# Kernel optimization log

Measured on AMD Instinct MI355X. Metric: run time of the kernel, lower is better.

## Reference

```python
import jax, jax.numpy as jnp
import numpy as np

EPS = 1e-5
HEADS = 8  # heads kwarg of TransformerDecoder


def _ln(x, g, b):
    mu = jnp.mean(x, axis=-1, keepdims=True)
    var = jnp.var(x, axis=-1, keepdims=True)
    return (x - mu) * jax.lax.rsqrt(var + EPS) * g + b


def _expert(params, xt, m, scale):
    """One TransformerDecoder expert (BIT-style): per layer, PreNorm2 cross-attn + residual,
    then PreNorm FeedForward + residual. xt: (B,S,D), m: (B,Nt,D)."""
    an_g, an_b, wq, wk, wv, wo, wo_b, fn_g, fn_b, w1, b1, w2, b2 = params
    L = an_g.shape[0]
    B, S, D = xt.shape
    Nt = m.shape[1]
    for l in range(L):
        xn = _ln(xt, an_g[l], an_b[l])
        mn = _ln(m, an_g[l], an_b[l])  # PreNorm2 norms both streams with the same LN
        q = (xn @ wq[l]).reshape(B, S, HEADS, -1)
        k = (mn @ wk[l]).reshape(B, Nt, HEADS, -1)
        v = (mn @ wv[l]).reshape(B, Nt, HEADS, -1)
        attn = jax.nn.softmax(jnp.einsum('bihd,bjhd->bhij', q, k) * scale, axis=-1)
        o = jnp.einsum('bhij,bjhd->bihd', attn, v).reshape(B, S, -1)
        xt = xt + o @ wo[l] + wo_b[l]
        h = _ln(xt, fn_g[l], fn_b[l])
        xt = xt + jax.nn.gelu(h @ w1[l] + b1[l], approximate=False) @ w2[l] + b2[l]
    return xt


def setup_inputs():
    key = jax.random.key(0)
    ks = iter(jax.random.split(key, 40))
    B, C, H, W = 4, 128, 64, 64
    D, INNER, FF, P, L, NT = 256, 512, 1024, 4, 2, 8
    r = lambda shape, s=1.0: jax.random.normal(next(ks), shape, jnp.float32) * s
    return {
        'x': r((B, C, H, W)),
        'm': r((B, NT, D)),
        'proj_w': r((C, D), 0.05), 'proj_b': r((D,), 0.02),
        'lnp_g': jnp.ones((D,), jnp.float32), 'lnp_b': jnp.zeros((D,), jnp.float32),
        'sq_w': r((D, D), 0.05), 'sq_b': r((D,), 0.02),
        'sk_w': r((D, D), 0.05), 'sk_b': r((D,), 0.02),
        'sv_w': r((D, 1), 0.05), 'sv_b': r((1,), 0.02),
        'an_g': jnp.ones((P, L, D), jnp.float32), 'an_b': jnp.zeros((P, L, D), jnp.float32),
        'wq': r((P, L, D, INNER), 0.05), 'wk': r((P, L, D, INNER), 0.05), 'wv': r((P, L, D, INNER), 0.05),
        'wo': r((P, L, INNER, D), 0.05), 'wo_b': r((P, L, D), 0.02),
        'fn_g': jnp.ones((P, L, D), jnp.float32), 'fn_b': jnp.zeros((P, L, D), jnp.float32),
        'w1': r((P, L, D, FF), 0.05), 'b1': r((P, L, FF), 0.02),
        'w2': r((P, L, FF, D), 0.05), 'b2': r((P, L, D), 0.02),
        'fln_g': jnp.ones((D,), jnp.float32), 'fln_b': jnp.zeros((D,), jnp.float32),
    }


def reference(x, m, proj_w, proj_b, lnp_g, lnp_b, sq_w, sq_b, sk_w, sk_b, sv_w, sv_b,
              an_g, an_b, wq, wk, wv, wo, wo_b, fn_g, fn_b, w1, b1, w2, b2, fln_g, fln_b):
    B, C, H, W = x.shape
    D = proj_w.shape[1]
    # 1x1 conv -> flatten(2).transpose(1,2): row-major (h,w) tokens
    tokens = jnp.einsum('bchw,cd->bhwd', x, proj_w).reshape(B, H * W, D) + proj_b
    tokens = _ln(tokens, lnp_g, lnp_b)
    # TokenScorer: cross-attention importance scores, v projects to scalar
    q = tokens @ sq_w + sq_b
    k = m @ sk_w + sk_b
    v = m @ sv_w + sv_b  # (B, Nt, 1)
    aw = jax.nn.softmax(jnp.einsum('bnd,bmd->bnm', q, k) / jnp.sqrt(jnp.float32(D)), axis=-1)
    scores = jnp.einsum('bnm,bmo->bno', aw, v)[..., 0]  # (B, N)
    P = an_g.shape[0]
    N = tokens.shape[1]
    S = N // P
    # descending sort of token scores
    idx = jnp.argsort(-scores, axis=1)  # (B, N)
    pscores = jnp.take_along_axis(scores, idx, axis=1).reshape(B, P, S).mean(-1)  # (B, P)
    pw = jax.nn.softmax(pscores, axis=1)  # (B, P)
    # gather tokens per partition: (P, B, S, D)
    gathered = jnp.take_along_axis(tokens, idx[..., None], axis=1).reshape(B, P, S, D).transpose(1, 0, 2, 3)
    scale = 1.0 / jnp.sqrt(jnp.float32(D))  # Cross_Attention scale = dim ** -0.5
    params = (an_g, an_b, wq, wk, wv, wo, wo_b, fn_g, fn_b, w1, b1, w2, b2)
    proc = jax.vmap(lambda pr, xt: _expert(pr, xt, m, scale))(params, gathered)  # (P, B, S, D)
    proc = proc * pw.T[:, :, None, None]
    flat = proc.transpose(1, 0, 2, 3).reshape(B, N, D)
    # scatter back into original token order (idx is a permutation)
    out = jnp.zeros_like(tokens).at[jnp.arange(B)[:, None], idx].set(flat)
    return _ln(out, fln_g, fln_b)
```

## Files before the change

### kernel.cpp

```cpp
#include <hip/hip_runtime.h>
#include <hip/hip_bf16.h>
#include <math.h>

#define BB 4
#define CC 128
#define NN 4096
#define DD 256
#define INNER 512
#define FFD 1024
#define PP 4
#define LL 2
#define NT 8
#define SS 1024
#define SCALE 0.0625f

typedef __attribute__((ext_vector_type(8))) short bf16x8;
typedef __attribute__((ext_vector_type(8))) short short8;
typedef __attribute__((ext_vector_type(4))) short short4v;
typedef __attribute__((ext_vector_type(4))) float f32x4;

#define GLD_LDS16(g, l) __builtin_amdgcn_global_load_lds( \
    (const __attribute__((address_space(1))) void*)(g), \
    (__attribute__((address_space(3))) void*)(l), 16, 0, 0)

template<int NW>
__device__ inline float block_sum(float v, float* sbuf){
  #pragma unroll
  for (int mk=32; mk; mk>>=1) v += __shfl_xor(v, mk);
  int w = threadIdx.x>>6;
  if ((threadIdx.x&63)==0) sbuf[w]=v;
  __syncthreads();
  float r = 0.f;
  #pragma unroll
  for (int k=0;k<NW;k++) r += sbuf[k];
  __syncthreads();
  return r;
}

__device__ inline unsigned short bf16bits(float v){
  __hip_bfloat16 t = __float2bfloat16(v);
  unsigned short u;
  __builtin_memcpy(&u, &t, 2);
  return u;
}
__device__ inline float bf2f(unsigned short u){
  unsigned int x = ((unsigned int)u)<<16;
  float f;
  __builtin_memcpy(&f, &x, 4);
  return f;
}

__device__ inline float gelu_f(float x){
  float z  = x * 0.70710678118654752440f;
  float az = fabsf(z);
  float t  = 1.0f / (1.0f + 0.3275911f*az);
  float y  = t*(0.254829592f + t*(-0.284496736f + t*(1.421413741f +
             t*(-1.453152027f + t*1.061405429f))));
  float erfv = 1.0f - y*__expf(-az*az);
  erfv = (z < 0.0f) ? -erfv : erfv;
  return 0.5f*x*(1.0f+erfv);
}

__global__ __launch_bounds__(256) void prep_kernel(
    const float* __restrict__ m, const float* __restrict__ sk_w,
    const float* __restrict__ sk_b, const float* __restrict__ sv_w,
    const float* __restrict__ sv_b, const float* __restrict__ sq_w,
    const float* __restrict__ sq_b,
    float* __restrict__ kk2, float* __restrict__ kb, float* __restrict__ vsc,
    const float* __restrict__ an_g, const float* __restrict__ an_b,
    const float* __restrict__ wk, const float* __restrict__ wv,
    float* __restrict__ kvk, float* __restrict__ kvv,
    const float* __restrict__ wq, const float* __restrict__ w1,
    const float* __restrict__ w2,
    __hip_bfloat16* __restrict__ wqT, __hip_bfloat16* __restrict__ w1T,
    __hip_bfloat16* __restrict__ w2T)
{
  __shared__ float smem[64*65];
  int z = blockIdx.x;
  int tid = threadIdx.x;
  if (z < 32){
    float* ms = smem;
    float* ks = smem + 256;
    float* sbuf = smem + 512;
    int bj = z;
    ms[tid] = m[bj*DD + tid];
    __syncthreads();
    float acc=0.f;
    #pragma unroll 8
    for(int c=0;c<DD;c++) acc = fmaf(ms[c], sk_w[c*DD + tid], acc);
    ks[tid] = acc + sk_b[tid];
    float sv = block_sum<4>(ms[tid]*sv_w[tid], sbuf);
    if(tid==0) vsc[bj] = sv + sv_b[0];
    __syncthreads();
    const float* wr = sq_w + (long)tid*DD;
    float a2 = 0.f;
    #pragma unroll 4
    for (int c=0; c<DD; c+=4){
      float4 wvv = *(const float4*)(wr + c);
      a2 = fmaf(wvv.x, ks[c+0], fmaf(wvv.y, ks[c+1], fmaf(wvv.z, ks[c+2], fmaf(wvv.w, ks[c+3], a2))));
    }
    kk2[bj*DD + tid] = a2;
    float kbv = block_sum<4>(sq_b[tid]*ks[tid], sbuf);
    if (tid==0) kb[bj] = kbv;
  } else if (z < 288){
    float* mn = smem;
    float* sbuf = smem + 256;
    int idx = z - 32;
    int j = idx & 7, b = (idx>>3)&3, pl = idx>>5;
    float v = m[(b*NT+j)*DD + tid];
    float s = block_sum<4>(v, sbuf);
    float mu = s*(1.0f/256.0f);
    float dv = v-mu;
    float q = block_sum<4>(dv*dv, sbuf);
    float rs = rsqrtf(q*(1.0f/256.0f)+1e-5f);
    mn[tid] = dv*rs*an_g[pl*DD+tid] + an_b[pl*DD+tid];
    __syncthreads();
    float ka0=0.f, va0=0.f, ka1=0.f, va1=0.f;
    const float* wkb = wk + (long)pl*DD*INNER;
    const float* wvb = wv + (long)pl*DD*INNER;
    #pragma unroll 8
    for (int c=0;c<DD;c++){
      float mc = mn[c];
      const float* wkr = wkb + (long)c*INNER;
      const float* wvr = wvb + (long)c*INNER;
      ka0 = fmaf(mc, wkr[tid], ka0);
      ka1 = fmaf(mc, wkr[tid+256], ka1);
      va0 = fmaf(mc, wvr[tid], va0);
      va1 = fmaf(mc, wvr[tid+256], va1);
    }
    long off = ((long)pl*BB + b)*(NT*INNER) + j*INNER;
    kvk[off+tid]=ka0; kvk[off+tid+256]=ka1;
    kvv[off+tid]=va0; kvv[off+tid+256]=va1;
  } else {
    int z2 = z - 288;
    const float* src; __hip_bfloat16* dst; int K, N, rel;
    if (z2 < 256)      { src=wq; dst=wqT; K=DD;   N=INNER; rel=z2; }
    else if (z2 < 768) { src=w1; dst=w1T; K=DD;   N=FFD;   rel=z2-256; }
    else               { src=w2; dst=w2T; K=FFD;  N=DD;    rel=z2-768; }
    int tn = N>>6, tk = K>>6, per = tn*tk;
    int pl = rel/per, r2 = rel%per;
    int n0 = (r2%tn)*64, k0 = (r2/tn)*64;
    float (*t)[65] = (float(*)[65])smem;
    #pragma unroll
    for (int i=0;i<4;i++){
      int idx = i*256+tid;
      int kk = idx>>4, n4 = idx&15;
      float4 v = *(const float4*)&src[((long)pl*K + k0+kk)*N + n0 + n4*4];
      t[kk][n4*4+0]=v.x; t[kk][n4*4+1]=v.y; t[kk][n4*4+2]=v.z; t[kk][n4*4+3]=v.w;
    }
    __syncthreads();
    #pragma unroll
    for (int i=0;i<4;i++){
      int idx = i*256+tid;
      int nn = idx>>4, k4 = idx&15;
      short4v o;
      o[0] = (short)bf16bits(t[k4*4+0][nn]);
      o[1] = (short)bf16bits(t[k4*4+1][nn]);
      o[2] = (short)bf16bits(t[k4*4+2][nn]);
      o[3] = (short)bf16bits(t[k4*4+3][nn]);
      *(short4v*)&dst[((long)pl*N + n0+nn)*K + k0 + k4*4] = o;
    }
  }
}

__global__ __launch_bounds__(256) void proj_ln_score_kernel(
    const float* __restrict__ x, const float* __restrict__ proj_w,
    const float* __restrict__ proj_b, const float* __restrict__ lnp_g,
    const float* __restrict__ lnp_b, const float* __restrict__ kk2,
    const float* __restrict__ kb, const float* __restrict__ vsc,
    float* __restrict__ tokens, float* __restrict__ scores,
    int* __restrict__ rank, long long* __restrict__ psumsI)
{
  int b  = blockIdx.x >> 8;
  int n0 = (blockIdx.x & 255) * 16;
  int tid = threadIdx.x;
  __shared__ float xs[16][132];
  __shared__ float ys[16][260];
  __shared__ float kj[8][260];
  __shared__ float kbs[8], vs[8];
  __shared__ float mu_s[16], rs_s[16];
  __shared__ float lg[16][8];
  if (tid < 16) rank[b*NN + n0 + tid] = 0;
  if (blockIdx.x == 0 && tid < 16) psumsI[tid] = 0;
  #pragma unroll
  for (int i=0;i<8;i++){
    int l = tid + i*256;
    int t = l & 15, c = l >> 4;
    xs[t][c] = x[(long)(b*CC + c)*NN + n0 + t];
  }
  #pragma unroll
  for (int i=0;i<8;i++){
    int idx = i*256 + tid;
    int r = idx >> 8, c = idx & 255;
    kj[r][c] = kk2[(b*NT + r)*DD + c];
  }
  if (tid < 8){ kbs[tid] = kb[b*NT+tid]; vs[tid] = vsc[b*NT+tid]; }
  __syncthreads();
  float acc[16];
  #pragma unroll
  for (int t=0;t<16;t++) acc[t]=0.f;
  for (int c0=0;c0<CC;c0+=4){
    float w0 = proj_w[(c0+0)*DD + tid];
    float w1_ = proj_w[(c0+1)*DD + tid];
    float w2_ = proj_w[(c0+2)*DD + tid];
    float w3_ = proj_w[(c0+3)*DD + tid];
    #pragma unroll
    for (int t=0;t<16;t++){
      float4 xv = *(const float4*)&xs[t][c0];
      acc[t] = fmaf(xv.x,w0,fmaf(xv.y,w1_,fmaf(xv.z,w2_,fmaf(xv.w,w3_,acc[t]))));
    }
  }
  float pb = proj_b[tid];
  #pragma unroll
  for (int t=0;t<16;t++) ys[t][tid] = acc[t] + pb;
  __syncthreads();
  int w = tid>>6, lane = tid&63;
  for (int k=0;k<4;k++){
    int t = w*4+k;
    float s = ys[t][lane] + ys[t][lane+64] + ys[t][lane+128] + ys[t][lane+192];
    #pragma unroll
    for (int mk=32; mk; mk>>=1) s += __shfl_xor(s, mk);
    float mu = s*(1.0f/256.0f);
    float d0=ys[t][lane]-mu, d1=ys[t][lane+64]-mu, d2=ys[t][lane+128]-mu, d3=ys[t][lane+192]-mu;
    float q = d0*d0+d1*d1+d2*d2+d3*d3;
    #pragma unroll
    for (int mk=32; mk; mk>>=1) q += __shfl_xor(q, mk);
    if (lane==0){ mu_s[t]=mu; rs_s[t]=rsqrtf(q*(1.0f/256.0f)+1e-5f); }
  }
  __syncthreads();
  float g = lnp_g[tid], be = lnp_b[tid];
  #pragma unroll
  for (int t=0;t<16;t++){
    float nv = (ys[t][tid]-mu_s[t])*rs_s[t]*g + be;
    tokens[((long)(b*NN + n0 + t))*DD + tid] = nv;
    ys[t][tid] = nv;
  }
  __syncthreads();
  if (tid < 128){
    int t = tid>>3, j = tid&7;
    float a2 = 0.f;
    for (int c0=0;c0<DD;c0+=4){
      float4 tv = *(const float4*)&ys[t][c0];
      float4 kv = *(const float4*)&kj[j][c0];
      a2 = fmaf(tv.x,kv.x,fmaf(tv.y,kv.y,fmaf(tv.z,kv.z,fmaf(tv.w,kv.w,a2))));
    }
    lg[t][j] = (a2 + kbs[j]) * SCALE;
  }
  __syncthreads();
  if (tid < 16){
    float mx=-1e30f;
    #pragma unroll
    for(int j=0;j<NT;j++) mx=fmaxf(mx,lg[tid][j]);
    float s=0.f, sc=0.f;
    #pragma unroll
    for(int j=0;j<NT;j++){ float e=__expf(lg[tid][j]-mx); s+=e; sc+=e*vs[j]; }
    scores[b*NN + n0 + tid] = sc/s;
  }
}

__global__ __launch_bounds__(256) void rank_partial_kernel(
    const float* __restrict__ scores, int* __restrict__ rank)
{
  int b  = blockIdx.x >> 8;
  int it = (blockIdx.x >> 4) & 15;
  int jt = blockIdx.x & 15;
  int i = it*256 + threadIdx.x;
  float si = scores[b*NN + i];
  __shared__ float ss[256];
  ss[threadIdx.x] = scores[b*NN + jt*256 + threadIdx.x];
  __syncthreads();
  int jbase = jt*256;
  int cnt = 0;
  #pragma unroll 4
  for (int j=0;j<256;j++){
    float sj = ss[j];
    cnt += (sj > si) || (sj == si && (jbase+j) < i);
  }
  atomicAdd(&rank[b*NN+i], cnt);
}

__global__ __launch_bounds__(256) void rank_finalize_kernel(
    const int* __restrict__ rank, const float* __restrict__ scores,
    int* __restrict__ cidx, long long* __restrict__ psumsI)
{
  __shared__ unsigned long long bins[PP];
  if (threadIdx.x < PP) bins[threadIdx.x] = 0ull;
  __syncthreads();
  int b = blockIdx.x >> 4;
  int i = (blockIdx.x & 15)*256 + threadIdx.x;
  int rk = rank[b*NN + i];
  int p = rk >> 10;
  cidx[(b*PP + p)*SS + (rk & (SS-1))] = i;
  long long iv = (long long)llrintf(scores[b*NN + i] * 268435456.0f);
  atomicAdd(&bins[p], (unsigned long long)iv);
  __syncthreads();
  if (threadIdx.x < PP)
    atomicAdd((unsigned long long*)&psumsI[b*PP + threadIdx.x], bins[threadIdx.x]);
}

__global__ __launch_bounds__(256) void gather_ln_kernel(
    const float* __restrict__ tokens, const int* __restrict__ cidx,
    float* __restrict__ Xc, __hip_bfloat16* __restrict__ Y,
    const float* __restrict__ gamma, const float* __restrict__ beta)
{
  long slot = (long)blockIdx.x*8 + (threadIdx.x>>5);
  int l32 = threadIdx.x & 31;
  int b = (int)(slot >> 12);
  int p = (int)((slot>>10)&3);
  int i = cidx[slot];
  const float* src = tokens + ((long)b*NN + i)*DD + l32*8;
  float4 v0 = *(const float4*)src;
  float4 v1 = *(const float4*)(src+4);
  *(float4*)(Xc + slot*DD + l32*8) = v0;
  *(float4*)(Xc + slot*DD + l32*8 + 4) = v1;
  float s = v0.x+v0.y+v0.z+v0.w+v1.x+v1.y+v1.z+v1.w;
  #pragma unroll
  for (int mk=16; mk; mk>>=1) s += __shfl_xor(s, mk);
  float mu = s*(1.0f/256.0f);
  float vv[8] = {v0.x,v0.y,v0.z,v0.w,v1.x,v1.y,v1.z,v1.w};
  float q = 0.f;
  #pragma unroll
  for (int k=0;k<8;k++){ float d = vv[k]-mu; q += d*d; }
  #pragma unroll
  for (int mk=16; mk; mk>>=1) q += __shfl_xor(q, mk);
  float rs = rsqrtf(q*(1.0f/256.0f)+1e-5f);
  short8 o;
  #pragma unroll
  for (int k=0;k<8;k++){
    int d = l32*8+k;
    o[k] = (short)bf16bits((vv[k]-mu)*rs*gamma[p*(LL*DD)+d]+beta[p*(LL*DD)+d]);
  }
  *(short8*)(Y + slot*DD + l32*8) = o;
}

__global__ __launch_bounds__(256) void qkvwo_kernel(
    const float* __restrict__ kvk, const float* __restrict__ kvv,
    const __hip_bfloat16* __restrict__ wqT, const float* __restrict__ wo,
    __hip_bfloat16* __restrict__ qkBuf, __hip_bfloat16* __restrict__ vwoT)
{
  int zz = blockIdx.x;
  int z = zz>>3, h = zz&7;
  int l = z>>4, g = z&15;
  int b = g>>2, p = g&3;
  int pl = p*LL + l;
  int c = threadIdx.x;
  __shared__ float kL[8][64];
  __shared__ float vL[8][64];
  {
    int j0 = c>>6, d0 = c&63;
    long off = ((long)pl*BB + b)*(NT*INNER) + h*64 + d0;
    kL[j0][d0]   = kvk[off + j0*INNER];
    vL[j0][d0]   = kvv[off + j0*INNER];
    kL[j0+4][d0] = kvk[off + (j0+4)*INNER];
    vL[j0+4][d0] = kvv[off + (j0+4)*INNER];
  }
  __syncthreads();
  float qa[8] = {0,0,0,0,0,0,0,0};
  float va[8] = {0,0,0,0,0,0,0,0};
  const __hip_bfloat16* wqp = wqT + ((long)pl*INNER + h*64)*DD + c;
  const float* wop = wo + ((long)pl*INNER + h*64)*DD + c;
  #pragma unroll 4
  for (int d=0; d<64; d++){
    float wqv = bf2f(*(const unsigned short*)(wqp + (long)d*DD));
    float wov = wop[(long)d*DD];
    #pragma unroll
    for (int j=0;j<8;j++){
      qa[j] = fmaf(kL[j][d], wqv, qa[j]);
      va[j] = fmaf(vL[j][d], wov, va[j]);
    }
  }
  __hip_bfloat16* qkg = qkBuf + (long)z*64*256;
  __hip_bfloat16* vwg = vwoT + (long)z*256*64;
  #pragma unroll
  for (int j=0;j<8;j++)
    qkg[(h*8+j)*256 + c] = __float2bfloat16(qa[j]*SCALE);
  short8 o;
  #pragma unroll
  for (int j=0;j<8;j++) o[j] = (short)bf16bits(va[j]);
  *(short8*)(vwg + c*64 + h*8) = o;
}

template<bool HASBIAS, bool GELU, bool ACCUM>
__global__ __launch_bounds__(256) void mfma_gemm(
    const __hip_bfloat16* __restrict__ A, long astride, int K,
    const __hip_bfloat16* __restrict__ BT, long bpstride,
    const float* __restrict__ bias, int bias_pstride,
    void* __restrict__ Cp, int ldc, long cstride)
{
  int g = blockIdx.z;
  int p = g & 3;
  const __hip_bfloat16* Ag = A  + (long)g*astride + (long)blockIdx.x*128*K;
  const __hip_bfloat16* Bg = BT + (long)p*bpstride + (long)blockIdx.y*128*K;
  const float* biasg = HASBIAS ? (bias + (long)p*bias_pstride) : nullptr;

  __shared__ __align__(16) __hip_bfloat16 Asm[2][128*64];
  __shared__ __align__(16) __hip_bfloat16 Bsm[2][128*64];

  int tid = threadIdx.x;
  int w = tid>>6, lane = tid&63;
  int wr = w>>1, wc = w&1;
  int lr = lane>>4, lc = lane&15;
  int ldsbase = tid & ~63;

  const __hip_bfloat16* aseg[4];
  const __hip_bfloat16* bseg[4];
  #pragma unroll
  for (int i=0;i<4;i++){
    int seg = i*256 + tid;
    int r = seg>>3, sl = seg&7;
    int sg = sl ^ (r&7);
    aseg[i] = Ag + (long)r*K + sg*8;
    bseg[i] = Bg + (long)r*K + sg*8;
  }

  f32x4 acc[4][4] = {};
  int nt = K >> 6;

  #define STAGE(buf) do { \
    _Pragma("unroll") \
    for (int i_=0;i_<4;i_++) \
      GLD_LDS16(aseg[i_], &Asm[buf][(i_*256 + ldsbase)*8]); \
    _Pragma("unroll") \
    for (int i_=0;i_<4;i_++) \
      GLD_LDS16(bseg[i_], &Bsm[buf][(i_*256 + ldsbase)*8]); \
    _Pragma("unroll") \
    for (int i_=0;i_<4;i_++){ aseg[i_] += 64; bseg[i_] += 64; } \
  } while(0)

  STAGE(0);
  asm volatile("s_waitcnt vmcnt(0)" ::: "memory");
  __syncthreads();

  for (int t=0; t<nt; t++){
    int cur = t & 1;
    if (t+1 < nt) STAGE(cur^1);
    #pragma unroll
    for (int kc=0;kc<2;kc++){
      bf16x8 af[4], bfr[4];
      #pragma unroll
      for (int mi=0;mi<4;mi++){
        int r = wr*64 + mi*16 + lc;
        int s = kc*4 + lr;
        af[mi] = *(const bf16x8*)(&Asm[cur][r*64 + (s ^ (r&7))*8]);
      }
      #pragma unroll
      for (int ni=0;ni<4;ni++){
        int r = wc*64 + ni*16 + lc;
        int s = kc*4 + lr;
        bfr[ni] = *(const bf16x8*)(&Bsm[cur][r*64 + (s ^ (r&7))*8]);
      }
      #pragma unroll
      for (int mi=0;mi<4;mi++)
        #pragma unroll
        for (int ni=0;ni<4;ni++)
          acc[mi][ni] = __builtin_amdgcn_mfma_f32_16x16x32_bf16(af[mi], bfr[ni], acc[mi][ni], 0, 0, 0);
    }
    if (t+1 < nt) asm volatile("s_waitcnt vmcnt(0)" ::: "memory");
    __syncthreads();
  }
  #undef STAGE

  if (ACCUM){
    float* Cg = (float*)Cp + (long)g*cstride;
    #pragma unroll
    for (int ni=0;ni<4;ni++){
      int col = blockIdx.y*128 + wc*64 + ni*16 + lc;
      float bv = HASBIAS ? biasg[col] : 0.0f;
      #pragma unroll
      for (int mi=0;mi<4;mi++){
        int row = blockIdx.x*128 + wr*64 + mi*16 + lr*4;
        #pragma unroll
        for (int j=0;j<4;j++){
          float v = acc[mi][ni][j] + bv;
          if (GELU) v = gelu_f(v);
          Cg[(long)(row+j)*ldc + col] += v;
        }
      }
    }
  } else {
    __hip_bfloat16* Cg = (__hip_bfloat16*)Cp + (long)g*cstride;
    #pragma unroll
    for (int ni=0;ni<4;ni++){
      int col = blockIdx.y*128 + wc*64 + ni*16 + lc;
      float bv = HASBIAS ? biasg[col] : 0.0f;
      #pragma unroll
      for (int mi=0;mi<4;mi++){
        int row = blockIdx.x*128 + wr*64 + mi*16 + lr*4;
        #pragma unroll
        for (int j=0;j<4;j++){
          float v = acc[mi][ni][j] + bv;
          if (GELU) v = gelu_f(v);
          Cg[(long)(row+j)*ldc + col] = __float2bfloat16(v);
        }
      }
    }
  }
}

template<bool LAST>
__global__ __launch_bounds__(256) void ff2_fused_kernel(
    const __hip_bfloat16* __restrict__ F,
    const __hip_bfloat16* __restrict__ w2l,
    const float* __restrict__ b2l,
    float* __restrict__ Xc,
    const float* __restrict__ g_ln,
    const float* __restrict__ b_ln,
    __hip_bfloat16* __restrict__ actOut,
    const int* __restrict__ cidx,
    const long long* __restrict__ psumsI,
    float* __restrict__ out)
{
  int rb = blockIdx.x;
  int g  = blockIdx.y;
  int p  = g & 3;
  const __hip_bfloat16* Ag = F + ((long)g*SS + rb*64)*FFD;
  const __hip_bfloat16* Bg = w2l + (long)p*((long)LL*DD*FFD);

  __shared__ __align__(16) __hip_bfloat16 As[2][64*64];
  __shared__ __align__(16) __hip_bfloat16 Bs[2][256*64];

  int tid = threadIdx.x;
  int w = tid>>6, lane = tid&63;
  int lr = lane>>4, lc = lane&15;
  int ldsbase = tid & ~63;

  const __hip_bfloat16* aseg[2];
  const __hip_bfloat16* bseg[8];
  #pragma unroll
  for (int i=0;i<2;i++){
    int seg = i*256 + tid;
    int r = seg>>3, sl = seg&7;
    aseg[i] = Ag + (long)r*FFD + (sl ^ (r&7))*8;
  }
  #pragma unroll
  for (int i=0;i<8;i++){
    int seg = i*256 + tid;
    int r = seg>>3, sl = seg&7;
    bseg[i] = Bg + (long)r*FFD + (sl ^ (r&7))*8;
  }

  f32x4 acc[4][4] = {};

  #define STAGE2(buf) do { \
    _Pragma("unroll") \
    for (int i_=0;i_<2;i_++) \
      GLD_LDS16(aseg[i_], &As[buf][(i_*256 + ldsbase)*8]); \
    _Pragma("unroll") \
    for (int i_=0;i_<8;i_++) \
      GLD_LDS16(bseg[i_], &Bs[buf][(i_*256 + ldsbase)*8]); \
    _Pragma("unroll") \
    for (int i_=0;i_<2;i_++) aseg[i_] += 64; \
    _Pragma("unroll") \
    for (int i_=0;i_<8;i_++) bseg[i_] += 64; \
  } while(0)

  STAGE2(0);
  asm volatile("s_waitcnt vmcnt(0)" ::: "memory");
  __syncthreads();

  for (int t=0; t<16; t++){
    int cur = t & 1;
    if (t+1 < 16) STAGE2(cur^1);
    #pragma unroll
    for (int kc=0;kc<2;kc++){
      bf16x8 af[4], bfr[4];
      #pragma unroll
      for (int mi=0;mi<4;mi++){
        int r = mi*16 + lc;
        int s = kc*4 + lr;
        af[mi] = *(const bf16x8*)(&As[cur][r*64 + (s ^ (r&7))*8]);
      }
      #pragma unroll
      for (int ni=0;ni<4;ni++){
        int c = w*64 + ni*16 + lc;
        int s = kc*4 + lr;
        bfr[ni] = *(const bf16x8*)(&Bs[cur][c*64 + (s ^ (c&7))*8]);
      }
      #pragma unroll
      for (int mi=0;mi<4;mi++)
        #pragma unroll
        for (int ni=0;ni<4;ni++)
          acc[mi][ni] = __builtin_amdgcn_mfma_f32_16x16x32_bf16(af[mi], bfr[ni], acc[mi][ni], 0, 0, 0);
    }
    if (t+1 < 16) asm volatile("s_waitcnt vmcnt(0)" ::: "memory");
    __syncthreads();
  }
  #undef STAGE2

  __syncthreads();
  float* pfl = (float*)&As[0][0];
  float* pfq = (float*)&As[0][0] + 256;
  float* Xg = Xc + (long)g*SS*DD + (long)rb*64*DD;

  float pwv = 1.0f;
  if (LAST){
    int b = g>>2;
    float ps[4];
    #pragma unroll
    for (int p2=0;p2<4;p2++)
      ps[p2] = (float)((double)psumsI[b*PP+p2] * (1.0/268435456.0/1024.0));
    float mxp = fmaxf(fmaxf(ps[0],ps[1]),fmaxf(ps[2],ps[3]));
    float e0=__expf(ps[0]-mxp), e1=__expf(ps[1]-mxp), e2=__expf(ps[2]-mxp), e3=__expf(ps[3]-mxp);
    float es = e0+e1+e2+e3;
    float ev = (p==0)?e0:(p==1)?e1:(p==2)?e2:e3;
    pwv = ev/es;
  }

  float srow[4][4], qrow[4][4];
  #pragma unroll
  for (int mi=0;mi<4;mi++)
    #pragma unroll
    for (int j=0;j<4;j++){ srow[mi][j]=0.f; qrow[mi][j]=0.f; }
  #pragma unroll
  for (int ni=0;ni<4;ni++){
    int col = w*64 + ni*16 + lc;
    float bv = b2l[p*(LL*DD) + col];
    #pragma unroll
    for (int mi=0;mi<4;mi++){
      int row = mi*16 + lr*4;
      #pragma unroll
      for (int j=0;j<4;j++){
        float v = Xg[(long)(row+j)*DD + col] + acc[mi][ni][j] + bv;
        if (!LAST) Xg[(long)(row+j)*DD + col] = v;
        if (LAST) v *= pwv;
        acc[mi][ni][j] = v;
        srow[mi][j] += v;
        qrow[mi][j] += v*v;
      }
    }
  }
  #pragma unroll
  for (int mi=0;mi<4;mi++)
    #pragma unroll
    for (int j=0;j<4;j++){
      float s2=srow[mi][j], q2=qrow[mi][j];
      s2 += __shfl_xor(s2,1); q2 += __shfl_xor(q2,1);
      s2 += __shfl_xor(s2,2); q2 += __shfl_xor(q2,2);
      s2 += __shfl_xor(s2,4); q2 += __shfl_xor(q2,4);
      s2 += __shfl_xor(s2,8); q2 += __shfl_xor(q2,8);
      srow[mi][j]=s2; qrow[mi][j]=q2;
    }
  if (lc==0){
    #pragma unroll
    for (int mi=0;mi<4;mi++)
      #pragma unroll
      for (int j=0;j<4;j++){
        int row = mi*16 + lr*4 + j;
        pfl[w*64+row] = srow[mi][j];
        pfq[w*64+row] = qrow[mi][j];
      }
  }
  __syncthreads();

  if (!LAST){
    __hip_bfloat16* Ya = actOut + ((long)g*SS + rb*64)*DD;
    const float* fg = g_ln + p*(LL*DD);
    const float* fb = b_ln + p*(LL*DD);
    #pragma unroll
    for (int mi=0;mi<4;mi++){
      #pragma unroll
      for (int j=0;j<4;j++){
        int row = mi*16 + lr*4 + j;
        float S = pfl[row] + pfl[64+row] + pfl[128+row] + pfl[192+row];
        float Q = pfq[row] + pfq[64+row] + pfq[128+row] + pfq[192+row];
        float mu = S*(1.0f/256.0f);
        float var = Q*(1.0f/256.0f) - mu*mu;
        float rs2 = rsqrtf(var + 1e-5f);
        #pragma unroll
        for (int ni=0;ni<4;ni++){
          int col = w*64 + ni*16 + lc;
          Ya[(long)row*DD + col] =
              __float2bfloat16((acc[mi][ni][j]-mu)*rs2*fg[col]+fb[col]);
        }
      }
    }
  } else {
    int b = g>>2;
    #pragma unroll
    for (int mi=0;mi<4;mi++){
      #pragma unroll
      for (int j=0;j<4;j++){
        int row = mi*16 + lr*4 + j;
        long slot = (long)g*SS + rb*64 + row;
        int i = cidx[slot];
        float S = pfl[row] + pfl[64+row] + pfl[128+row] + pfl[192+row];
        float Q = pfq[row] + pfq[64+row] + pfq[128+row] + pfq[192+row];
        float mu = S*(1.0f/256.0f);
        float var = Q*(1.0f/256.0f) - mu*mu;
        float rs2 = rsqrtf(var + 1e-5f);
        float* op = out + ((long)b*NN + i)*DD;
        #pragma unroll
        for (int ni=0;ni<4;ni++){
          int col = w*64 + ni*16 + lc;
          op[col] = (acc[mi][ni][j]-mu)*rs2*g_ln[col]+b_ln[col];
        }
      }
    }
  }
}

__global__ __launch_bounds__(256) void fused_attn_kernel(
    const __hip_bfloat16* __restrict__ actA,
    const __hip_bfloat16* __restrict__ qk,
    const __hip_bfloat16* __restrict__ vwo,
    const float* __restrict__ wo_bl,
    const float* __restrict__ fn_gl,
    const float* __restrict__ fn_bl,
    float* __restrict__ Xc,
    __hip_bfloat16* __restrict__ actOut)
{
  int rb = blockIdx.x;
  int g  = blockIdx.y;
  int p  = g & 3;
  const __hip_bfloat16* Ag = actA + ((long)g*SS + rb*64)*DD;
  const __hip_bfloat16* Qg = qk  + (long)g*64*256;
  const __hip_bfloat16* Vg = vwo + (long)g*256*64;

  __shared__ __align__(16) __hip_bfloat16 sm[24576];
  int tid = threadIdx.x;
  int w = tid>>6, lane = tid&63;
  int lr = lane>>4, lc = lane&15;
  int ldsbase = tid & ~63;

  #pragma unroll
  for (int i=0;i<8;i++){
    int seg = i*256 + tid;
    int r = seg>>5, sl = seg&31;
    int sg = sl ^ (r&7);
    GLD_LDS16(Qg + (long)r*256 + sg*8, &sm[8192 + (i*256 + ldsbase)*8]);
  }
  #pragma unroll
  for (int i=0;i<2;i++){
    int seg = i*256 + tid;
    int r = seg>>3, sl = seg&7;
    int sg = sl ^ (r&7);
    GLD_LDS16(Ag + (long)r*DD + sg*8, &sm[0 + (i*256 + ldsbase)*8]);
  }
  asm volatile("s_waitcnt vmcnt(0)" ::: "memory");
  __syncthreads();

  f32x4 acc1[4] = {};
  for (int t=0; t<4; t++){
    int cur = t&1;
    if (t+1 < 4){
      #pragma unroll
      for (int i=0;i<2;i++){
        int seg = i*256 + tid;
        int r = seg>>3, sl = seg&7;
        int sg = sl ^ (r&7);
        GLD_LDS16(Ag + (long)r*DD + (t+1)*64 + sg*8,
                  &sm[(cur^1)*4096 + (i*256 + ldsbase)*8]);
      }
    }
    #pragma unroll
    for (int kc=0;kc<2;kc++){
      int r = w*16 + lc;
      int s = kc*4 + lr;
      bf16x8 af = *(const bf16x8*)(&sm[cur*4096 + r*64 + (s ^ (r&7))*8]);
      #pragma unroll
      for (int ni=0;ni<4;ni++){
        int rb_ = ni*16 + lc;
        int sb = t*8 + kc*4 + lr;
        bf16x8 bfr = *(const bf16x8*)(&sm[8192 + rb_*256 + (sb ^ (rb_&7))*8]);
        acc1[ni] = __builtin_amdgcn_mfma_f32_16x16x32_bf16(af, bfr, acc1[ni], 0, 0, 0);
      }
    }
    if (t+1 < 4) asm volatile("s_waitcnt vmcnt(0)" ::: "memory");
    __syncthreads();
  }

  #pragma unroll
  for (int i=0;i<8;i++){
    int seg = i*256 + tid;
    int r = seg>>3, sl = seg&7;
    int sg = sl ^ (r&7);
    GLD_LDS16(Vg + (long)r*64 + sg*8, &sm[8192 + (i*256 + ldsbase)*8]);
  }

  float pv[4][4];
  #pragma unroll
  for (int ni=0;ni<4;ni++){
    #pragma unroll
    for (int j=0;j<4;j++){
      float v = acc1[ni][j];
      float mx = v;
      mx = fmaxf(mx, __shfl_xor(mx,1));
      mx = fmaxf(mx, __shfl_xor(mx,2));
      mx = fmaxf(mx, __shfl_xor(mx,4));
      float e = __expf(v - mx);
      float ssum = e;
      ssum += __shfl_xor(ssum,1);
      ssum += __shfl_xor(ssum,2);
      ssum += __shfl_xor(ssum,4);
      pv[ni][j] = e / ssum;
    }
  }
  #pragma unroll
  for (int ni=0;ni<4;ni++){
    #pragma unroll
    for (int j=0;j<4;j++){
      int row = w*16 + lr*4 + j;
      int col = ni*16 + lc;
      int s = col>>3, e = col&7;
      sm[row*64 + ((s ^ (row&7))<<3) + e] = __float2bfloat16(pv[ni][j]);
    }
  }
  asm volatile("s_waitcnt vmcnt(0)" ::: "memory");
  __syncthreads();

  f32x4 acc2[4][4] = {};
  #pragma unroll
  for (int kc=0;kc<2;kc++){
    bf16x8 af[4], bfr[4];
    #pragma unroll
    for (int mi=0;mi<4;mi++){
      int r = mi*16 + lc;
      int s = kc*4 + lr;
      af[mi] = *(const bf16x8*)(&sm[r*64 + (s ^ (r&7))*8]);
    }
    #pragma unroll
    for (int ni=0;ni<4;ni++){
      int rb_ = w*64 + ni*16 + lc;
      int s = kc*4 + lr;
      bfr[ni] = *(const bf16x8*)(&sm[8192 + rb_*64 + (s ^ (rb_&7))*8]);
    }
    #pragma unroll
    for (int mi=0;mi<4;mi++)
      #pragma unroll
      for (int ni=0;ni<4;ni++)
        acc2[mi][ni] = __builtin_amdgcn_mfma_f32_16x16x32_bf16(af[mi], bfr[ni], acc2[mi][ni], 0, 0, 0);
  }

  __syncthreads();
  float* pfl = (float*)sm;
  float* pfq = (float*)sm + 256;
  float* Xg = Xc + (long)g*SS*DD + (long)rb*64*DD;
  float srow[4][4], qrow[4][4];
  #pragma unroll
  for (int mi=0;mi<4;mi++)
    #pragma unroll
    for (int j=0;j<4;j++){ srow[mi][j]=0.f; qrow[mi][j]=0.f; }
  #pragma unroll
  for (int ni=0;ni<4;ni++){
    int col = w*64 + ni*16 + lc;
    float bv = wo_bl[p*(LL*DD) + col];
    #pragma unroll
    for (int mi=0;mi<4;mi++){
      int row = mi*16 + lr*4;
      #pragma unroll
      for (int j=0;j<4;j++){
        float v = Xg[(long)(row+j)*DD + col] + acc2[mi][ni][j] + bv;
        Xg[(long)(row+j)*DD + col] = v;
        acc2[mi][ni][j] = v;
        srow[mi][j] += v;
        qrow[mi][j] += v*v;
      }
    }
  }
  #pragma unroll
  for (int mi=0;mi<4;mi++)
    #pragma unroll
    for (int j=0;j<4;j++){
      float s2=srow[mi][j], q2=qrow[mi][j];
      s2 += __shfl_xor(s2,1); q2 += __shfl_xor(q2,1);
      s2 += __shfl_xor(s2,2); q2 += __shfl_xor(q2,2);
      s2 += __shfl_xor(s2,4); q2 += __shfl_xor(q2,4);
      s2 += __shfl_xor(s2,8); q2 += __shfl_xor(q2,8);
      srow[mi][j]=s2; qrow[mi][j]=q2;
    }
  if (lc==0){
    #pragma unroll
    for (int mi=0;mi<4;mi++)
      #pragma unroll
      for (int j=0;j<4;j++){
        int row = mi*16 + lr*4 + j;
        pfl[w*64+row] = srow[mi][j];
        pfq[w*64+row] = qrow[mi][j];
      }
  }
  __syncthreads();
  __hip_bfloat16* Ya = actOut + ((long)g*SS + rb*64)*DD;
  const float* fg = fn_gl + p*(LL*DD);
  const float* fb = fn_bl + p*(LL*DD);
  #pragma unroll
  for (int mi=0;mi<4;mi++){
    #pragma unroll
    for (int j=0;j<4;j++){
      int row = mi*16 + lr*4 + j;
      float S = pfl[row] + pfl[64+row] + pfl[128+row] + pfl[192+row];
      float Q = pfq[row] + pfq[64+row] + pfq[128+row] + pfq[192+row];
      float mu = S*(1.0f/256.0f);
      float var = Q*(1.0f/256.0f) - mu*mu;
      float rs2 = rsqrtf(var + 1e-5f);
      #pragma unroll
      for (int ni=0;ni<4;ni++){
        int col = w*64 + ni*16 + lc;
        Ya[(long)row*DD + col] =
            __float2bfloat16((acc2[mi][ni][j]-mu)*rs2*fg[col]+fb[col]);
      }
    }
  }
}

extern "C" void kernel_launch(void* const* d_in, const int* in_sizes, int n_in,
                              void* d_out, int out_size, void* d_ws, size_t ws_size,
                              hipStream_t stream)
{
  (void)in_sizes; (void)n_in; (void)out_size; (void)ws_size;
  const float* x     =(const float*)d_in[0];
  const float* m     =(const float*)d_in[1];
  const float* proj_w=(const float*)d_in[2];
  const float* proj_b=(const float*)d_in[3];
  const float* lnp_g =(const float*)d_in[4];
  const float* lnp_b =(const float*)d_in[5];
  const float* sq_w  =(const float*)d_in[6];
  const float* sq_b  =(const float*)d_in[7];
  const float* sk_w  =(const float*)d_in[8];
  const float* sk_b  =(const float*)d_in[9];
  const float* sv_w  =(const float*)d_in[10];
  const float* sv_b  =(const float*)d_in[11];
  const float* an_g  =(const float*)d_in[12];
  const float* an_b  =(const float*)d_in[13];
  const float* wq    =(const float*)d_in[14];
  const float* wk    =(const float*)d_in[15];
  const float* wv    =(const float*)d_in[16];
  const float* wo    =(const float*)d_in[17];
  const float* wo_b  =(const float*)d_in[18];
  const float* fn_g  =(const float*)d_in[19];
  const float* fn_b  =(const float*)d_in[20];
  const float* w1    =(const float*)d_in[21];
  const float* b1    =(const float*)d_in[22];
  const float* w2    =(const float*)d_in[23];
  const float* b2    =(const float*)d_in[24];
  const float* fln_g =(const float*)d_in[25];
  const float* fln_b =(const float*)d_in[26];
  float* out = (float*)d_out;

  float* ws = (float*)d_ws;
  float* tokens  = ws;  ws += 4194304;
  ws += 4194304;
  float* Xc      = ws;  ws += 4194304;
  float* actAf   = ws;  ws += 2097152;
  float* wqTf    = ws;  ws += 524288;
  float* w1Tf    = ws;  ws += 1048576;
  float* w2Tf    = ws;  ws += 1048576;
  float* qkBf    = ws;  ws += 262144;
  float* vwoTf   = ws;  ws += 262144;
  float* kvk     = ws;  ws += 131072;
  float* kvv     = ws;  ws += 131072;
  float* kk2     = ws;  ws += 8192;
  float* kb      = ws;  ws += 32;
  float* vsc     = ws;  ws += 64;
  float* scores  = ws;  ws += 16384;
  long long* psumsI = (long long*)ws;  ws += 32;
  int* rank      = (int*)ws;  ws += 16384;
  int* cidx      = (int*)ws;  ws += 16384;

  __hip_bfloat16* actA  = (__hip_bfloat16*)actAf;
  __hip_bfloat16* actF  = (__hip_bfloat16*)tokens;
  __hip_bfloat16* wqT   = (__hip_bfloat16*)wqTf;
  __hip_bfloat16* w1T   = (__hip_bfloat16*)w1Tf;
  __hip_bfloat16* w2T   = (__hip_bfloat16*)w2Tf;
  __hip_bfloat16* qkBuf = (__hip_bfloat16*)qkBf;
  __hip_bfloat16* vwoT  = (__hip_bfloat16*)vwoTf;

  prep_kernel<<<1568,256,0,stream>>>(m, sk_w, sk_b, sv_w, sv_b, sq_w, sq_b,
                                     kk2, kb, vsc, an_g, an_b, wk, wv, kvk, kvv,
                                     wq, w1, w2, wqT, w1T, w2T);
  proj_ln_score_kernel<<<1024,256,0,stream>>>(x, proj_w, proj_b, lnp_g, lnp_b,
                                              kk2, kb, vsc, tokens, scores,
                                              rank, psumsI);
  rank_partial_kernel<<<1024,256,0,stream>>>(scores, rank);
  rank_finalize_kernel<<<64,256,0,stream>>>(rank, scores, cidx, psumsI);
  qkvwo_kernel<<<256,256,0,stream>>>(kvk, kvv, wqT, wo, qkBuf, vwoT);
  gather_ln_kernel<<<2048,256,0,stream>>>(tokens, cidx, Xc, actA, an_g, an_b);

  fused_attn_kernel<<<dim3(16,16),256,0,stream>>>(
      actA, qkBuf, vwoT, wo_b, fn_g, fn_b, Xc, actA);
  mfma_gemm<true,true,false><<<dim3(8,8,16),256,0,stream>>>(
      actA, (long)SS*DD, DD, w1T, (long)LL*FFD*DD,
      b1, LL*FFD, actF, FFD, (long)SS*FFD);
  ff2_fused_kernel<false><<<dim3(16,16),256,0,stream>>>(
      actF, w2T, b2, Xc, an_g + DD, an_b + DD, actA,
      nullptr, nullptr, nullptr);
  fused_attn_kernel<<<dim3(16,16),256,0,stream>>>(
      actA, qkBuf + (long)16*64*256, vwoT + (long)16*256*64,
      wo_b + DD, fn_g + DD, fn_b + DD, Xc, actA);
  mfma_gemm<true,true,false><<<dim3(8,8,16),256,0,stream>>>(
      actA, (long)SS*DD, DD, w1T + (long)FFD*DD, (long)LL*FFD*DD,
      b1 + FFD, LL*FFD, actF, FFD, (long)SS*FFD);
  ff2_fused_kernel<true><<<dim3(16,16),256,0,stream>>>(
      actF, w2T + (long)DD*FFD, b2 + DD, Xc, fln_g, fln_b, nullptr,
      cidx, psumsI, out);
}
```

Baseline: 245.8 us.

## Merge independent prep stages into shared launches to overlap small kernels

The scorer part is split out into its own small kernel. The projection/LN/score work is merged with the K/V projection and weight-transpose blocks into one launch, and rank counting is merged with the qk/vwo precompute into another. The goal is to cut launch count and let small, independent workloads run on idle CUs alongside each other, at the cost of a union shared-memory footprint sized for the largest branch. Only independent stages are merged, so dependencies are preserved.

```diff
diff --git a/kernel.cpp b/kernel.cpp
--- a/kernel.cpp
+++ b/kernel.cpp
@@ -61,51 +61,158 @@
   return 0.5f*x*(1.0f+erfv);
 }
 
-__global__ __launch_bounds__(256) void prep_kernel(
+__global__ __launch_bounds__(256) void scorer_kernel(
     const float* __restrict__ m, const float* __restrict__ sk_w,
     const float* __restrict__ sk_b, const float* __restrict__ sv_w,
     const float* __restrict__ sv_b, const float* __restrict__ sq_w,
     const float* __restrict__ sq_b,
-    float* __restrict__ kk2, float* __restrict__ kb, float* __restrict__ vsc,
-    const float* __restrict__ an_g, const float* __restrict__ an_b,
-    const float* __restrict__ wk, const float* __restrict__ wv,
-    float* __restrict__ kvk, float* __restrict__ kvv,
+    float* __restrict__ kk2, float* __restrict__ kb, float* __restrict__ vsc)
+{
+  __shared__ float ms[256];
+  __shared__ float ks[256];
+  __shared__ float sbuf[4];
+  int bj = blockIdx.x;
+  int tid = threadIdx.x;
+  ms[tid] = m[bj*DD + tid];
+  __syncthreads();
+  float acc=0.f;
+  #pragma unroll 8
+  for(int c=0;c<DD;c++) acc = fmaf(ms[c], sk_w[c*DD + tid], acc);
+  ks[tid] = acc + sk_b[tid];
+  float sv = block_sum<4>(ms[tid]*sv_w[tid], sbuf);
+  if(tid==0) vsc[bj] = sv + sv_b[0];
+  __syncthreads();
+  const float* wr = sq_w + (long)tid*DD;
+  float a2 = 0.f;
+  #pragma unroll 4
+  for (int c=0; c<DD; c+=4){
+    float4 wvv = *(const float4*)(wr + c);
+    a2 = fmaf(wvv.x, ks[c+0], fmaf(wvv.y, ks[c+1], fmaf(wvv.z, ks[c+2], fmaf(wvv.w, ks[c+3], a2))));
+  }
+  kk2[bj*DD + tid] = a2;
+  float kbv = block_sum<4>(sq_b[tid]*ks[tid], sbuf);
+  if (tid==0) kb[bj] = kbv;
+}
+
+__global__ __launch_bounds__(256) void proj_prep_kernel(
+    const float* __restrict__ x, const float* __restrict__ proj_w,
+    const float* __restrict__ proj_b, const float* __restrict__ lnp_g,
+    const float* __restrict__ lnp_b, const float* __restrict__ kk2,
+    const float* __restrict__ kb, const float* __restrict__ vsc,
+    float* __restrict__ tokens, float* __restrict__ scores,
+    int* __restrict__ rank, long long* __restrict__ psumsI,
+    const float* __restrict__ m, const float* __restrict__ an_g,
+    const float* __restrict__ an_b, const float* __restrict__ wk,
+    const float* __restrict__ wv, float* __restrict__ kvk,
+    float* __restrict__ kvv,
     const float* __restrict__ wq, const float* __restrict__ w1,
     const float* __restrict__ w2,
     __hip_bfloat16* __restrict__ wqT, __hip_bfloat16* __restrict__ w1T,
     __hip_bfloat16* __restrict__ w2T)
 {
-  __shared__ float smem[64*65];
+  __shared__ union {
+    struct {
+      float xs[16][132];
+      float ys[16][260];
+      float kj[8][260];
+      float kbs[8], vs[8], mu_s[16], rs_s[16];
+      float lg[16][8];
+    } pr;
+    struct { float t[64][65]; } wc;
+    struct { float mn[256]; float sbuf[4]; } kv;
+  } sm;
   int z = blockIdx.x;
   int tid = threadIdx.x;
-  if (z < 32){
-    float* ms = smem;
-    float* ks = smem + 256;
-    float* sbuf = smem + 512;
-    int bj = z;
-    ms[tid] = m[bj*DD + tid];
-    __syncthreads();
-    float acc=0.f;
-    #pragma unroll 8
-    for(int c=0;c<DD;c++) acc = fmaf(ms[c], sk_w[c*DD + tid], acc);
-    ks[tid] = acc + sk_b[tid];
-    float sv = block_sum<4>(ms[tid]*sv_w[tid], sbuf);
-    if(tid==0) vsc[bj] = sv + sv_b[0];
-    __syncthreads();
-    const float* wr = sq_w + (long)tid*DD;
-    float a2 = 0.f;
-    #pragma unroll 4
-    for (int c=0; c<DD; c+=4){
-      float4 wvv = *(const float4*)(wr + c);
-      a2 = fmaf(wvv.x, ks[c+0], fmaf(wvv.y, ks[c+1], fmaf(wvv.z, ks[c+2], fmaf(wvv.w, ks[c+3], a2))));
-    }
-    kk2[bj*DD + tid] = a2;
-    float kbv = block_sum<4>(sq_b[tid]*ks[tid], sbuf);
-    if (tid==0) kb[bj] = kbv;
-  } else if (z < 288){
-    float* mn = smem;
-    float* sbuf = smem + 256;
-    int idx = z - 32;
+
+  if (z < 1024){
+    int b  = z >> 8;
+    int n0 = (z & 255) * 16;
+    if (tid < 16) rank[b*NN + n0 + tid] = 0;
+    if (z == 0 && tid < 16) psumsI[tid] = 0;
+    float (*xs)[132] = sm.pr.xs;
+    float (*ys)[260] = sm.pr.ys;
+    float (*kj)[260] = sm.pr.kj;
+    float* kbs = sm.pr.kbs; float* vs = sm.pr.vs;
+    float* mu_s = sm.pr.mu_s; float* rs_s = sm.pr.rs_s;
+    float (*lg)[8] = sm.pr.lg;
+    #pragma unroll
+    for (int i=0;i<8;i++){
+      int l = tid + i*256;
+      int t = l & 15, c = l >> 4;
+      xs[t][c] = x[(long)(b*CC + c)*NN + n0 + t];
+    }
+    #pragma unroll
+    for (int i=0;i<8;i++){
+      int idx = i*256 + tid;
+      int r = idx >> 8, c = idx & 255;
+      kj[r][c] = kk2[(b*NT + r)*DD + c];
+    }
+    if (tid < 8){ kbs[tid] = kb[b*NT+tid]; vs[tid] = vsc[b*NT+tid]; }
+    __syncthreads();
+    float acc[16];
+    #pragma unroll
+    for (int t=0;t<16;t++) acc[t]=0.f;
+    for (int c0=0;c0<CC;c0+=4){
+      float w0 = proj_w[(c0+0)*DD + tid];
+      float w1_ = proj_w[(c0+1)*DD + tid];
+      float w2_ = proj_w[(c0+2)*DD + tid];
+      float w3_ = proj_w[(c0+3)*DD + tid];
+      #pragma unroll
+      for (int t=0;t<16;t++){
+        float4 xv = *(const float4*)&xs[t][c0];
+        acc[t] = fmaf(xv.x,w0,fmaf(xv.y,w1_,fmaf(xv.z,w2_,fmaf(xv.w,w3_,acc[t]))));
+      }
+    }
+    float pb = proj_b[tid];
+    #pragma unroll
+    for (int t=0;t<16;t++) ys[t][tid] = acc[t] + pb;
+    __syncthreads();
+    int w = tid>>6, lane = tid&63;
+    for (int k=0;k<4;k++){
+      int t = w*4+k;
+      float s = ys[t][lane] + ys[t][lane+64] + ys[t][lane+128] + ys[t][lane+192];
+      #pragma unroll
+      for (int mk=32; mk; mk>>=1) s += __shfl_xor(s, mk);
+      float mu = s*(1.0f/256.0f);
+      float d0=ys[t][lane]-mu, d1=ys[t][lane+64]-mu, d2=ys[t][lane+128]-mu, d3=ys[t][lane+192]-mu;
+      float q = d0*d0+d1*d1+d2*d2+d3*d3;
+      #pragma unroll
+      for (int mk=32; mk; mk>>=1) q += __shfl_xor(q, mk);
+      if (lane==0){ mu_s[t]=mu; rs_s[t]=rsqrtf(q*(1.0f/256.0f)+1e-5f); }
+    }
+    __syncthreads();
+    float g = lnp_g[tid], be = lnp_b[tid];
+    #pragma unroll
+    for (int t=0;t<16;t++){
+      float nv = (ys[t][tid]-mu_s[t])*rs_s[t]*g + be;
+      tokens[((long)(b*NN + n0 + t))*DD + tid] = nv;
+      ys[t][tid] = nv;
+    }
+    __syncthreads();
+    if (tid < 128){
+      int t = tid>>3, j = tid&7;
+      float a2 = 0.f;
+      for (int c0=0;c0<DD;c0+=4){
+        float4 tv = *(const float4*)&ys[t][c0];
+        float4 kv2 = *(const float4*)&kj[j][c0];
+        a2 = fmaf(tv.x,kv2.x,fmaf(tv.y,kv2.y,fmaf(tv.z,kv2.z,fmaf(tv.w,kv2.w,a2))));
+      }
+      lg[t][j] = (a2 + kbs[j]) * SCALE;
+    }
+    __syncthreads();
+    if (tid < 16){
+      float mx=-1e30f;
+      #pragma unroll
+      for(int j=0;j<NT;j++) mx=fmaxf(mx,lg[tid][j]);
+      float s=0.f, sc=0.f;
+      #pragma unroll
+      for(int j=0;j<NT;j++){ float e=__expf(lg[tid][j]-mx); s+=e; sc+=e*vs[j]; }
+      scores[b*NN + n0 + tid] = sc/s;
+    }
+  } else if (z < 1280){
+    float* mn = sm.kv.mn;
+    float* sbuf = sm.kv.sbuf;
+    int idx = z - 1024;
     int j = idx & 7, b = (idx>>3)&3, pl = idx>>5;
     float v = m[(b*NT+j)*DD + tid];
     float s = block_sum<4>(v, sbuf);
@@ -132,7 +239,7 @@
     kvk[off+tid]=ka0; kvk[off+tid+256]=ka1;
     kvv[off+tid]=va0; kvv[off+tid+256]=va1;
   } else {
-    int z2 = z - 288;
+    int z2 = z - 1280;
     const float* src; __hip_bfloat16* dst; int K, N, rel;
     if (z2 < 256)      { src=wq; dst=wqT; K=DD;   N=INNER; rel=z2; }
     else if (z2 < 768) { src=w1; dst=w1T; K=DD;   N=FFD;   rel=z2-256; }
@@ -140,7 +247,7 @@
     int tn = N>>6, tk = K>>6, per = tn*tk;
     int pl = rel/per, r2 = rel%per;
     int n0 = (r2%tn)*64, k0 = (r2/tn)*64;
-    float (*t)[65] = (float(*)[65])smem;
+    float (*t)[65] = sm.wc.t;
     #pragma unroll
     for (int i=0;i<4;i++){
       int idx = i*256+tid;
@@ -163,120 +270,75 @@
   }
 }
 
-__global__ __launch_bounds__(256) void proj_ln_score_kernel(
-    const float* __restrict__ x, const float* __restrict__ proj_w,
-    const float* __restrict__ proj_b, const float* __restrict__ lnp_g,
-    const float* __restrict__ lnp_b, const float* __restrict__ kk2,
-    const float* __restrict__ kb, const float* __restrict__ vsc,
-    float* __restrict__ tokens, float* __restrict__ scores,
-    int* __restrict__ rank, long long* __restrict__ psumsI)
+__global__ __launch_bounds__(256) void rank_qkvwo_kernel(
+    const float* __restrict__ scores, int* __restrict__ rank,
+    const float* __restrict__ kvk, const float* __restrict__ kvv,
+    const __hip_bfloat16* __restrict__ wqT, const float* __restrict__ wo,
+    __hip_bfloat16* __restrict__ qkBuf, __hip_bfloat16* __restrict__ vwoT)
 {
-  int b  = blockIdx.x >> 8;
-  int n0 = (blockIdx.x & 255) * 16;
-  int tid = threadIdx.x;
-  __shared__ float xs[16][132];
-  __shared__ float ys[16][260];
-  __shared__ float kj[8][260];
-  __shared__ float kbs[8], vs[8];
-  __shared__ float mu_s[16], rs_s[16];
-  __shared__ float lg[16][8];
-  if (tid < 16) rank[b*NN + n0 + tid] = 0;
-  if (blockIdx.x == 0 && tid < 16) psumsI[tid] = 0;
-  #pragma unroll
-  for (int i=0;i<8;i++){
-    int l = tid + i*256;
-    int t = l & 15, c = l >> 4;
-    xs[t][c] = x[(long)(b*CC + c)*NN + n0 + t];
-  }
-  #pragma unroll
-  for (int i=0;i<8;i++){
-    int idx = i*256 + tid;
-    int r = idx >> 8, c = idx & 255;
-    kj[r][c] = kk2[(b*NT + r)*DD + c];
-  }
-  if (tid < 8){ kbs[tid] = kb[b*NT+tid]; vs[tid] = vsc[b*NT+tid]; }
-  __syncthreads();
-  float acc[16];
-  #pragma unroll
-  for (int t=0;t<16;t++) acc[t]=0.f;
-  for (int c0=0;c0<CC;c0+=4){
-    float w0 = proj_w[(c0+0)*DD + tid];
-    float w1_ = proj_w[(c0+1)*DD + tid];
-    float w2_ = proj_w[(c0+2)*DD + tid];
-    float w3_ = proj_w[(c0+3)*DD + tid];
-    #pragma unroll
-    for (int t=0;t<16;t++){
-      float4 xv = *(const float4*)&xs[t][c0];
-      acc[t] = fmaf(xv.x,w0,fmaf(xv.y,w1_,fmaf(xv.z,w2_,fmaf(xv.w,w3_,acc[t]))));
-    }
-  }
-  float pb = proj_b[tid];
-  #pragma unroll
-  for (int t=0;t<16;t++) ys[t][tid] = acc[t] + pb;
-  __syncthreads();
-  int w = tid>>6, lane = tid&63;
-  for (int k=0;k<4;k++){
-    int t = w*4+k;
-    float s = ys[t][lane] + ys[t][lane+64] + ys[t][lane+128] + ys[t][lane+192];
-    #pragma unroll
-    for (int mk=32; mk; mk>>=1) s += __shfl_xor(s, mk);
-    float mu = s*(1.0f/256.0f);
-    float d0=ys[t][lane]-mu, d1=ys[t][lane+64]-mu, d2=ys[t][lane+128]-mu, d3=ys[t][lane+192]-mu;
-    float q = d0*d0+d1*d1+d2*d2+d3*d3;
-    #pragma unroll
-    for (int mk=32; mk; mk>>=1) q += __shfl_xor(q, mk);
-    if (lane==0){ mu_s[t]=mu; rs_s[t]=rsqrtf(q*(1.0f/256.0f)+1e-5f); }
-  }
-  __syncthreads();
-  float g = lnp_g[tid], be = lnp_b[tid];
-  #pragma unroll
-  for (int t=0;t<16;t++){
-    float nv = (ys[t][tid]-mu_s[t])*rs_s[t]*g + be;
-    tokens[((long)(b*NN + n0 + t))*DD + tid] = nv;
-    ys[t][tid] = nv;
-  }
-  __syncthreads();
-  if (tid < 128){
-    int t = tid>>3, j = tid&7;
-    float a2 = 0.f;
-    for (int c0=0;c0<DD;c0+=4){
-      float4 tv = *(const float4*)&ys[t][c0];
-      float4 kv = *(const float4*)&kj[j][c0];
-      a2 = fmaf(tv.x,kv.x,fmaf(tv.y,kv.y,fmaf(tv.z,kv.z,fmaf(tv.w,kv.w,a2))));
-    }
-    lg[t][j] = (a2 + kbs[j]) * SCALE;
-  }
-  __syncthreads();
-  if (tid < 16){
-    float mx=-1e30f;
-    #pragma unroll
-    for(int j=0;j<NT;j++) mx=fmaxf(mx,lg[tid][j]);
-    float s=0.f, sc=0.f;
-    #pragma unroll
-    for(int j=0;j<NT;j++){ float e=__expf(lg[tid][j]-mx); s+=e; sc+=e*vs[j]; }
-    scores[b*NN + n0 + tid] = sc/s;
-  }
-}
-
-__global__ __launch_bounds__(256) void rank_partial_kernel(
-    const float* __restrict__ scores, int* __restrict__ rank)
-{
-  int b  = blockIdx.x >> 8;
-  int it = (blockIdx.x >> 4) & 15;
-  int jt = blockIdx.x & 15;
-  int i = it*256 + threadIdx.x;
-  float si = scores[b*NN + i];
-  __shared__ float ss[256];
-  ss[threadIdx.x] = scores[b*NN + jt*256 + threadIdx.x];
-  __syncthreads();
-  int jbase = jt*256;
-  int cnt = 0;
-  #pragma unroll 4
-  for (int j=0;j<256;j++){
-    float sj = ss[j];
-    cnt += (sj > si) || (sj == si && (jbase+j) < i);
-  }
-  atomicAdd(&rank[b*NN+i], cnt);
+  __shared__ union {
+    struct { float ss[256]; } rk;
+    struct { float kL[8][64]; float vL[8][64]; } qv;
+  } sm;
+  int z = blockIdx.x;
+  if (z < 1024){
+    int b  = z >> 8;
+    int it = (z >> 4) & 15;
+    int jt = z & 15;
+    int i = it*256 + threadIdx.x;
+    float si = scores[b*NN + i];
+    sm.rk.ss[threadIdx.x] = scores[b*NN + jt*256 + threadIdx.x];
+    __syncthreads();
+    int jbase = jt*256;
+    int cnt = 0;
+    #pragma unroll 4
+    for (int j=0;j<256;j++){
+      float sj = sm.rk.ss[j];
+      cnt += (sj > si) || (sj == si && (jbase+j) < i);
+    }
+    atomicAdd(&rank[b*NN+i], cnt);
+  } else {
+    int zz = z - 1024;
+    int z3 = zz>>3, h = zz&7;
+    int l = z3>>4, g = z3&15;
+    int b = g>>2, p = g&3;
+    int pl = p*LL + l;
+    int c = threadIdx.x;
+    float (*kL)[64] = sm.qv.kL;
+    float (*vL)[64] = sm.qv.vL;
+    {
+      int j0 = c>>6, d0 = c&63;
+      long off = ((long)pl*BB + b)*(NT*INNER) + h*64 + d0;
+      kL[j0][d0]   = kvk[off + j0*INNER];
+      vL[j0][d0]   = kvv[off + j0*INNER];
+      kL[j0+4][d0] = kvk[off + (j0+4)*INNER];
+      vL[j0+4][d0] = kvv[off + (j0+4)*INNER];
+    }
+    __syncthreads();
+    float qa[8] = {0,0,0,0,0,0,0,0};
+    float va[8] = {0,0,0,0,0,0,0,0};
+    const __hip_bfloat16* wqp = wqT + ((long)pl*INNER + h*64)*DD + c;
+    const float* wop = wo + ((long)pl*INNER + h*64)*DD + c;
+    #pragma unroll 4
+    for (int d=0; d<64; d++){
+      float wqv = bf2f(*(const unsigned short*)(wqp + (long)d*DD));
+      float wov = wop[(long)d*DD];
+      #pragma unroll
+      for (int j=0;j<8;j++){
+        qa[j] = fmaf(kL[j][d], wqv, qa[j]);
+        va[j] = fmaf(vL[j][d], wov, va[j]);
+      }
+    }
+    __hip_bfloat16* qkg = qkBuf + (long)z3*64*256;
+    __hip_bfloat16* vwg = vwoT + (long)z3*256*64;
+    #pragma unroll
+    for (int j=0;j<8;j++)
+      qkg[(h*8+j)*256 + c] = __float2bfloat16(qa[j]*SCALE);
+    short8 o;
+    #pragma unroll
+    for (int j=0;j<8;j++) o[j] = (short)bf16bits(va[j]);
+    *(short8*)(vwg + c*64 + h*8) = o;
+  }
 }
 
 __global__ __launch_bounds__(256) void rank_finalize_kernel(
@@ -331,53 +393,6 @@
     o[k] = (short)bf16bits((vv[k]-mu)*rs*gamma[p*(LL*DD)+d]+beta[p*(LL*DD)+d]);
   }
   *(short8*)(Y + slot*DD + l32*8) = o;
-}
-
-__global__ __launch_bounds__(256) void qkvwo_kernel(
-    const float* __restrict__ kvk, const float* __restrict__ kvv,
-    const __hip_bfloat16* __restrict__ wqT, const float* __restrict__ wo,
-    __hip_bfloat16* __restrict__ qkBuf, __hip_bfloat16* __restrict__ vwoT)
-{
-  int zz = blockIdx.x;
-  int z = zz>>3, h = zz&7;
-  int l = z>>4, g = z&15;
-  int b = g>>2, p = g&3;
-  int pl = p*LL + l;
-  int c = threadIdx.x;
-  __shared__ float kL[8][64];
-  __shared__ float vL[8][64];
-  {
-    int j0 = c>>6, d0 = c&63;
-    long off = ((long)pl*BB + b)*(NT*INNER) + h*64 + d0;
-    kL[j0][d0]   = kvk[off + j0*INNER];
-    vL[j0][d0]   = kvv[off + j0*INNER];
-    kL[j0+4][d0] = kvk[off + (j0+4)*INNER];
-    vL[j0+4][d0] = kvv[off + (j0+4)*INNER];
-  }
-  __syncthreads();
-  float qa[8] = {0,0,0,0,0,0,0,0};
-  float va[8] = {0,0,0,0,0,0,0,0};
-  const __hip_bfloat16* wqp = wqT + ((long)pl*INNER + h*64)*DD + c;
-  const float* wop = wo + ((long)pl*INNER + h*64)*DD + c;
-  #pragma unroll 4
-  for (int d=0; d<64; d++){
-    float wqv = bf2f(*(const unsigned short*)(wqp + (long)d*DD));
-    float wov = wop[(long)d*DD];
-    #pragma unroll
-    for (int j=0;j<8;j++){
-      qa[j] = fmaf(kL[j][d], wqv, qa[j]);
-      va[j] = fmaf(vL[j][d], wov, va[j]);
-    }
-  }
-  __hip_bfloat16* qkg = qkBuf + (long)z*64*256;
-  __hip_bfloat16* vwg = vwoT + (long)z*256*64;
-  #pragma unroll
-  for (int j=0;j<8;j++)
-    qkg[(h*8+j)*256 + c] = __float2bfloat16(qa[j]*SCALE);
-  short8 o;
-  #pragma unroll
-  for (int j=0;j<8;j++) o[j] = (short)bf16bits(va[j]);
-  *(short8*)(vwg + c*64 + h*8) = o;
 }
 
 template<bool HASBIAS, bool GELU, bool ACCUM>
@@ -964,15 +979,16 @@
   __hip_bfloat16* qkBuf = (__hip_bfloat16*)qkBf;
   __hip_bfloat16* vwoT  = (__hip_bfloat16*)vwoTf;
 
-  prep_kernel<<<1568,256,0,stream>>>(m, sk_w, sk_b, sv_w, sv_b, sq_w, sq_b,
-                                     kk2, kb, vsc, an_g, an_b, wk, wv, kvk, kvv,
-                                     wq, w1, w2, wqT, w1T, w2T);
-  proj_ln_score_kernel<<<1024,256,0,stream>>>(x, proj_w, proj_b, lnp_g, lnp_b,
-                                              kk2, kb, vsc, tokens, scores,
-                                              rank, psumsI);
-  rank_partial_kernel<<<1024,256,0,stream>>>(scores, rank);
+  scorer_kernel<<<32,256,0,stream>>>(m, sk_w, sk_b, sv_w, sv_b, sq_w, sq_b,
+                                     kk2, kb, vsc);
+  proj_prep_kernel<<<2560,256,0,stream>>>(
+      x, proj_w, proj_b, lnp_g, lnp_b, kk2, kb, vsc,
+      tokens, scores, rank, psumsI,
+      m, an_g, an_b, wk, wv, kvk, kvv,
+      wq, w1, w2, wqT, w1T, w2T);
+  rank_qkvwo_kernel<<<1280,256,0,stream>>>(scores, rank, kvk, kvv, wqT, wo,
+                                           qkBuf, vwoT);
   rank_finalize_kernel<<<64,256,0,stream>>>(rank, scores, cidx, psumsI);
-  qkvwo_kernel<<<256,256,0,stream>>>(kvk, kvv, wqT, wo, qkBuf, vwoT);
   gather_ln_kernel<<<2048,256,0,stream>>>(tokens, cidx, Xc, actA, an_g, an_b);
 
   fused_attn_kernel<<<dim3(16,16),256,0,stream>>>(
```

After: 244.7 us. Within noise of the previous version (-0.5%).
